# Kernel tuning notes

Measured on AMD Instinct MI355X. Metric: run time of the kernel, lower is better.

Reference implementation:

```python
import jax, jax.numpy as jnp
import numpy as np

B, J, D, W, H, EH, L = 128, 8192, 32, 4, 128, 256, 32
TEMP = 1.0


def _ln(x, g, b, eps=1e-5):
    mu = jnp.mean(x, axis=-1, keepdims=True)
    var = jnp.var(x, axis=-1, keepdims=True)
    return (x - mu) * jax.lax.rsqrt(var + eps) * g + b


def setup_inputs() -> dict:
    key = jax.random.key(0)
    ks = jax.random.split(key, 12)

    def lin(k, fi, fo):
        k1, k2 = jax.random.split(k)
        s = 1.0 / np.sqrt(fi)
        return (jax.random.uniform(k1, (fi, fo), minval=-s, maxval=s, dtype=jnp.float32),
                jax.random.uniform(k2, (fo,), minval=-s, maxval=s, dtype=jnp.float32))

    h_w1, h_b1 = lin(ks[0], 1 + D, H)
    h_w2, h_b2 = lin(ks[1], H, D)
    g_w1, g_b1 = lin(ks[2], D, D // 2)
    g_w2, g_b2 = lin(ks[3], D // 2, W)
    c_w, c_b = lin(ks[4], W * D, D)
    e_w1, e_b1 = lin(ks[5], D, EH)
    e_w2, e_b2 = lin(ks[6], EH, 2 * L)
    return {
        'x': jax.random.normal(ks[7], (B, J), dtype=jnp.float32),
        'mask': jax.random.randint(ks[8], (B, J), 0, 2, dtype=jnp.int32),
        'fe': jax.random.normal(ks[9], (J, D), dtype=jnp.float32),
        'h_w1': h_w1, 'h_b1': h_b1,
        'h_ln1_w': jnp.ones((H,), jnp.float32), 'h_ln1_b': jnp.zeros((H,), jnp.float32),
        'h_w2': h_w2, 'h_b2': h_b2,
        'h_ln2_w': jnp.ones((D,), jnp.float32), 'h_ln2_b': jnp.zeros((D,), jnp.float32),
        'g_w1': g_w1, 'g_b1': g_b1, 'g_w2': g_w2, 'g_b2': g_b2,
        'c_w': c_w, 'c_b': c_b,
        'c_ln_w': jnp.ones((D,), jnp.float32), 'c_ln_b': jnp.zeros((D,), jnp.float32),
        'e_w1': e_w1, 'e_b1': e_b1,
        'e_ln1_w': jnp.ones((EH,), jnp.float32), 'e_ln1_b': jnp.zeros((EH,), jnp.float32),
        'e_w2': e_w2, 'e_b2': e_b2,
        'e_ln2_w': jnp.ones((2 * L,), jnp.float32), 'e_ln2_b': jnp.zeros((2 * L,), jnp.float32),
    }


def _forward(x, mask, fe, h_w1, h_b1, h_ln1_w, h_ln1_b, h_w2, h_b2, h_ln2_w, h_ln2_b,
             g_w1, g_b1, g_w2, g_b2, c_w, c_b, c_ln_w, c_ln_b,
             e_w1, e_b1, e_ln1_w, e_ln1_b, e_w2, e_b2, e_ln2_w, e_ln2_b):
    relu = jax.nn.relu
    # h_in = concat([x, F]) @ h_w1 split into scalar column + shared embedding part
    # (fe @ h_w1[1:]) is [J,H], shared across cells -> avoids materializing [B,J,1+D]
    pre = x[..., None] * h_w1[0][None, None, :] + (fe @ h_w1[1:])[None] + h_b1  # [B,J,H]
    h1 = relu(_ln(pre, h_ln1_w, h_ln1_b))
    h_out = relu(_ln(h1 @ h_w2 + h_b2, h_ln2_w, h_ln2_b))  # [B,J,D]
    raw_gates = relu(h_out @ g_w1 + g_b1) @ g_w2 + g_b2  # [B,J,W]
    logits = jnp.clip(raw_gates * TEMP, -10.0, 10.0)
    logits = jnp.where(mask[..., None] > 0, logits, -1e9)  # masked gather -> -inf fill
    weights = jax.nn.softmax(logits, axis=1)  # softmax over observed junctions
    head_sums = jnp.einsum('bjw,bjd->bwd', weights, h_out)  # [B,W,D]
    comb = relu(_ln(head_sums.reshape(head_sums.shape[0], -1) @ c_w + c_b, c_ln_w, c_ln_b))
    comb = jnp.where((jnp.sum(mask, axis=1) > 0)[:, None], comb, 0.0)  # zero cells -> zeros
    h = relu(_ln(comb @ e_w1 + e_b1, e_ln1_w, e_ln1_b))
    o = relu(_ln(h @ e_w2 + e_b2, e_ln2_w, e_ln2_b))
    mu, logvar = jnp.split(o, 2, axis=-1)
    return mu, logvar


def reference(x, mask, fe, h_w1, h_b1, h_ln1_w, h_ln1_b, h_w2, h_b2, h_ln2_w, h_ln2_b,
              g_w1, g_b1, g_w2, g_b2, c_w, c_b, c_ln_w, c_ln_b,
              e_w1, e_b1, e_ln1_w, e_ln1_b, e_w2, e_b2, e_ln2_w, e_ln2_b):
    return _forward(x, mask, fe, h_w1, h_b1, h_ln1_w, h_ln1_b, h_w2, h_b2, h_ln2_w, h_ln2_b,
                    g_w1, g_b1, g_w2, g_b2, c_w, c_b, c_ln_w, c_ln_b,
                    e_w1, e_b1, e_ln1_w, e_ln1_b, e_w2, e_b2, e_ln2_w, e_ln2_b)
```

## Files before the change

### kernel.cpp

```cpp
#include <hip/hip_runtime.h>
#include <cstdint>

#define BDIM 128
#define JDIM 8192

typedef short s8x __attribute__((ext_vector_type(8)));
typedef float f4x __attribute__((ext_vector_type(4)));
typedef float f2x __attribute__((ext_vector_type(2)));

__device__ __forceinline__ unsigned short bf16u(float f) {
    return __builtin_bit_cast(unsigned short, (__bf16)f);
}
__device__ __forceinline__ unsigned int pkbf(float lo, float hi) {
    return (unsigned int)bf16u(lo) | ((unsigned int)bf16u(hi) << 16);
}
__device__ __forceinline__ f2x upk(unsigned int w) {
    f2x r;
    r.x = __uint_as_float(w << 16);
    r.y = __uint_as_float(w & 0xffff0000u);
    return r;
}
__device__ __forceinline__ f2x pkfma(f2x a, f2x b, f2x c) {
    return __builtin_elementwise_fma(a, b, c);
}
__device__ __forceinline__ f2x pkmax0(f2x a) {
    f2x z = {0.f, 0.f};
    return __builtin_elementwise_max(a, z);
}

__device__ __forceinline__ float allred16(float x) {
    float t;
    asm("v_add_f32 %0, %1, %1 quad_perm:[1,0,3,2] row_mask:0xf bank_mask:0xf"
        : "=v"(t) : "v"(x));
    asm("v_add_f32 %0, %1, %1 quad_perm:[2,3,0,1] row_mask:0xf bank_mask:0xf"
        : "=v"(x) : "v"(t));
    asm("v_add_f32 %0, %1, %1 row_half_mirror row_mask:0xf bank_mask:0xf"
        : "=v"(t) : "v"(x));
    asm("v_add_f32 %0, %1, %1 row_mirror row_mask:0xf bank_mask:0xf"
        : "=v"(x) : "v"(t));
    return x;
}

__global__ __launch_bounds__(128) void k_prep(
    const float* __restrict__ fe, const float* __restrict__ hw1,
    const float* __restrict__ hb1,
    const float* __restrict__ hw2, const float* __restrict__ gw1,
    unsigned short* __restrict__ feWb, float* __restrict__ aux,
    float* __restrict__ scal, uint4* __restrict__ fragW)
{
    const int h = threadIdx.x;
    __shared__ float red[2][3];
    const int wv = h >> 6, ln = h & 63;
    float w1r[32];
#pragma unroll
    for (int d = 0; d < 32; ++d) w1r[d] = hw1[(1 + d) * 128 + h];
    const float hb = hb1[h];
    const float w0h = hw1[h];

    for (int q = 0; q < 8; ++q) {
        const int j = blockIdx.x * 8 + q;
        float acc = hb;
#pragma unroll
        for (int d = 0; d < 32; ++d) acc = fmaf(fe[j * 32 + d], w1r[d], acc);
        feWb[(size_t)j * 128 + h] = bf16u(acc);

        float s1 = acc, sx = w0h * acc, s2 = acc * acc;
#pragma unroll
        for (int m = 1; m <= 32; m <<= 1) {
            s1 += __shfl_xor(s1, m); sx += __shfl_xor(sx, m); s2 += __shfl_xor(s2, m);
        }
        if (q) __syncthreads();
        if (ln == 0) { red[wv][0] = s1; red[wv][1] = sx; red[wv][2] = s2; }
        __syncthreads();
        if (h == 0) {
            aux[j * 4 + 0] = (red[0][0] + red[1][0]) * (1.f / 128.f);
            aux[j * 4 + 1] = (red[0][1] + red[1][1]) * (1.f / 128.f);
            aux[j * 4 + 2] = (red[0][2] + red[1][2]) * (1.f / 128.f);
        }
    }

    if (blockIdx.x == 0) {
        float a = w0h, b = w0h * w0h;
#pragma unroll
        for (int m = 1; m <= 32; m <<= 1) { a += __shfl_xor(a, m); b += __shfl_xor(b, m); }
        __syncthreads();
        if (ln == 0) { red[wv][0] = a; red[wv][1] = b; }
        __syncthreads();
        if (h == 0) {
            scal[0] = (red[0][0] + red[1][0]) * (1.f / 128.f);
            scal[1] = (red[0][1] + red[1][1]) * (1.f / 128.f);
        }
        if (h < 64) {
            const int cc = h & 15, gg = h >> 4;
#pragma unroll
            for (int nt = 0; nt < 2; ++nt)
#pragma unroll
                for (int t = 0; t < 4; ++t) {
                    const int kb = 32 * t + 8 * gg, n = 16 * nt + cc;
                    uint4 u;
                    u.x = pkbf(hw2[(kb + 0) * 32 + n], hw2[(kb + 1) * 32 + n]);
                    u.y = pkbf(hw2[(kb + 2) * 32 + n], hw2[(kb + 3) * 32 + n]);
                    u.z = pkbf(hw2[(kb + 4) * 32 + n], hw2[(kb + 5) * 32 + n]);
                    u.w = pkbf(hw2[(kb + 6) * 32 + n], hw2[(kb + 7) * 32 + n]);
                    fragW[(nt * 4 + t) * 64 + h] = u;
                }
            uint4 u;
            u.x = pkbf(gw1[(8 * gg + 0) * 16 + cc], gw1[(8 * gg + 1) * 16 + cc]);
            u.y = pkbf(gw1[(8 * gg + 2) * 16 + cc], gw1[(8 * gg + 3) * 16 + cc]);
            u.z = pkbf(gw1[(8 * gg + 4) * 16 + cc], gw1[(8 * gg + 5) * 16 + cc]);
            u.w = pkbf(gw1[(8 * gg + 6) * 16 + cc], gw1[(8 * gg + 7) * 16 + cc]);
            fragW[8 * 64 + h] = u;
        }
    }
}

template <int JPW>
__global__ __launch_bounds__(256, 2) void k_main(
    const float* __restrict__ x, const int* __restrict__ mask,
    const unsigned short* __restrict__ feWb, const float* __restrict__ aux,
    const float* __restrict__ scal, const uint4* __restrict__ fragW,
    const float* __restrict__ hw1, const float* __restrict__ ln1w,
    const float* __restrict__ ln1b,
    const float* __restrict__ hb2,
    const float* __restrict__ ln2w, const float* __restrict__ ln2b,
    const float* __restrict__ gb1,
    const float* __restrict__ gw2, const float* __restrict__ gb2,
    float* __restrict__ P, float* __restrict__ SEb, int njb)
{
    __shared__ float w0s[128], g1s[128], b1s[128];
    __shared__ float holds[8][576];
    __shared__ float hsL[2048];
    __shared__ float seL[64];

    const int tid = threadIdx.x, l = tid & 63;
    const int wv = __builtin_amdgcn_readfirstlane(tid >> 6);
    const int c = l & 15, g = l >> 4;
    const int bt = blockIdx.y, bx = blockIdx.x;
    const int b0 = bt * 16;

    if (tid < 128) { w0s[tid] = hw1[tid]; g1s[tid] = ln1w[tid]; b1s[tid] = ln1b[tid]; }
    __syncthreads();

    const float mw0 = scal[0], q0 = scal[1];

    s8x wf[2][4];
#pragma unroll
    for (int nt = 0; nt < 2; ++nt)
#pragma unroll
        for (int t = 0; t < 4; ++t)
            wf[nt][t] = __builtin_bit_cast(s8x, fragW[(nt * 4 + t) * 64 + l]);
    const s8x g1f = __builtin_bit_cast(s8x, fragW[8 * 64 + l]);

    const float hb2a = hb2[c],      hb2b = hb2[16 + c];
    const float g2a  = ln2w[c],     g2b  = ln2w[16 + c];
    const float z2a  = ln2b[c],     z2b  = ln2b[16 + c];
    const float gb1c = gb1[c];
    const float L2E  = 1.442695040888963f;
    float gw2c[4], gb2l[4];
#pragma unroll
    for (int w = 0; w < 4; ++w) {
        gw2c[w] = gw2[c * 4 + w];
        gb2l[w] = fmaf(gb2[w], L2E, -10.f * L2E);
    }

    const int j0 = (bx * 4 + wv) * JPW;
    const float* xrow = x + (size_t)(b0 + c) * JDIM;
    const int*   mrow = mask + (size_t)(b0 + c) * JDIM;

    f2x   hsacc[4][4];
    float seacc[4][4];
#pragma unroll
    for (int r = 0; r < 4; ++r)
#pragma unroll
        for (int w = 0; w < 4; ++w) {
            hsacc[r][w].x = 0.f; hsacc[r][w].y = 0.f; seacc[r][w] = 0.f;
        }

    for (int jp = 0; jp < JPW / 2; ++jp) {
        const int jb = j0 + jp * 2;

        float xv[2], rsv[2], nms[2]; int mv[2];
#pragma unroll
        for (int p = 0; p < 2; ++p) {
            xv[p] = xrow[jb + p];
            mv[p] = mrow[jb + p];
            const float4 au = *(const float4*)(aux + (size_t)(jb + p) * 4);
            const float mu = fmaf(xv[p], mw0, au.x);
            const float e2 = fmaf(xv[p] * xv[p], q0, fmaf(2.f * xv[p], au.y, au.z));
            rsv[p] = rsqrtf(e2 - mu * mu + 1e-5f);
            nms[p] = -mu * rsv[p];
        }

        f4x ca[2], cb[2];
#pragma unroll
        for (int p = 0; p < 2; ++p) { ca[p] = f4x{0.f,0.f,0.f,0.f}; cb[p] = f4x{0.f,0.f,0.f,0.f}; }
#pragma unroll
        for (int p = 0; p < 2; ++p) {
            const f2x xv2 = {xv[p], xv[p]}, rs2 = {rsv[p], rsv[p]}, nm2 = {nms[p], nms[p]};
            const unsigned short* fj = feWb + (size_t)(jb + p) * 128;
#pragma unroll
            for (int t = 0; t < 4; ++t) {
                const int kb = 32 * t + 8 * g;
                const uint4 fw = *(const uint4*)(fj + kb);
                const unsigned int fwv[4] = {fw.x, fw.y, fw.z, fw.w};
                const f2x* wp = (const f2x*)&w0s[kb];
                const f2x* gp = (const f2x*)&g1s[kb];
                const f2x* bp = (const f2x*)&b1s[kb];
                unsigned int res[4];
#pragma unroll
                for (int q = 0; q < 4; ++q) {
                    f2x h2 = pkfma(xv2, wp[q], upk(fwv[q]));
                    h2 = pkfma(h2, rs2, nm2);
                    h2 = pkfma(h2, gp[q], bp[q]);
                    h2 = pkmax0(h2);
                    res[q] = pkbf(h2.x, h2.y);
                }
                const uint4 u = make_uint4(res[0], res[1], res[2], res[3]);
                const s8x af = __builtin_bit_cast(s8x, u);
                ca[p] = __builtin_amdgcn_mfma_f32_16x16x32_bf16(af, wf[0][t], ca[p], 0, 0, 0);
                cb[p] = __builtin_amdgcn_mfma_f32_16x16x32_bf16(af, wf[1][t], cb[p], 0, 0, 0);
            }
        }

        float ho0[2][4], ho1[2][4];
#pragma unroll
        for (int p = 0; p < 2; ++p) {
            float v0[4], v1[4], sr[4], qr[4];
#pragma unroll
            for (int r = 0; r < 4; ++r) {
                v0[r] = ca[p][r] + hb2a;
                v1[r] = cb[p][r] + hb2b;
                sr[r] = v0[r] + v1[r];
                qr[r] = v0[r] * v0[r] + v1[r] * v1[r];
            }
#pragma unroll
            for (int r = 0; r < 4; ++r) { sr[r] = allred16(sr[r]); qr[r] = allred16(qr[r]); }
#pragma unroll
            for (int r = 0; r < 4; ++r) {
                const float m2   = sr[r] * 0.03125f;
                const float rs2b = rsqrtf(fmaf(qr[r], 0.03125f, -m2 * m2) + 1e-5f);
                const float nm2b = -m2 * rs2b;
                ho0[p][r] = fmaxf(fmaf(fmaf(v0[r], rs2b, nm2b), g2a, z2a), 0.f);
                ho1[p][r] = fmaxf(fmaf(fmaf(v1[r], rs2b, nm2b), g2b, z2b), 0.f);
            }
        }

#pragma unroll
        for (int p = 0; p < 2; ++p) {
            float* hp = &holds[wv * 2 + p][0];
#pragma unroll
            for (int r = 0; r < 4; ++r) {
                hp[(4 * g + r) * 36 + c]      = ho0[p][r];
                hp[(4 * g + r) * 36 + 16 + c] = ho1[p][r];
            }
        }
        asm volatile("s_waitcnt lgkmcnt(0)" ::: "memory");
        f4x gc[2];
#pragma unroll
        for (int p = 0; p < 2; ++p) {
            const float* hp = &holds[wv * 2 + p][0];
            const float4 ra  = *(const float4*)&hp[c * 36 + 8 * g];
            const float4 rb2 = *(const float4*)&hp[c * 36 + 8 * g + 4];
            uint4 ua;
            ua.x = pkbf(ra.x, ra.y);   ua.y = pkbf(ra.z, ra.w);
            ua.z = pkbf(rb2.x, rb2.y); ua.w = pkbf(rb2.z, rb2.w);
            const s8x af2 = __builtin_bit_cast(s8x, ua);
            f4x z = {0.f, 0.f, 0.f, 0.f};
            gc[p] = __builtin_amdgcn_mfma_f32_16x16x32_bf16(af2, g1f, z, 0, 0, 0);
        }

#pragma unroll
        for (int p = 0; p < 2; ++p) {
            float pw[16];
#pragma unroll
            for (int r = 0; r < 4; ++r) {
                const float g1r = fmaxf(gc[p][r] + gb1c, 0.f);
#pragma unroll
                for (int w = 0; w < 4; ++w) pw[r * 4 + w] = g1r * gw2c[w];
            }
#pragma unroll
            for (int i = 0; i < 16; ++i) pw[i] = allred16(pw[i]);

            const unsigned bm = (unsigned)__ballot(mv[p] > 0);
            float fm[4];
#pragma unroll
            for (int r = 0; r < 4; ++r) fm[r] = (float)((bm >> (4 * g + r)) & 1u);

#pragma unroll
            for (int r = 0; r < 4; ++r) {
                const f2x ho2 = {ho0[p][r], ho1[p][r]};
#pragma unroll
                for (int w = 0; w < 4; ++w) {
                    float t = fmaf(pw[r * 4 + w], L2E, gb2l[w]);
                    t = __builtin_amdgcn_fmed3f(t, -20.f * L2E, 0.f);
                    const float e = fm[r] * __builtin_amdgcn_exp2f(t);
                    seacc[r][w] += e;
                    const f2x e2v = {e, e};
                    hsacc[r][w] = pkfma(e2v, ho2, hsacc[r][w]);
                }
            }
        }
    }

    for (int ww = 0; ww < 4; ++ww) {
        __syncthreads();
        if (wv == ww) {
#pragma unroll
            for (int r = 0; r < 4; ++r)
#pragma unroll
                for (int w = 0; w < 4; ++w)
#pragma unroll
                    for (int nt = 0; nt < 2; ++nt) {
                        const int idx = ((4 * g + r) * 4 + w) * 32 + c + 16 * nt;
                        const float val = nt ? hsacc[r][w].y : hsacc[r][w].x;
                        if (ww == 0) hsL[idx] = val;
                        else         hsL[idx] += val;
                    }
            if (c == 0) {
#pragma unroll
                for (int r = 0; r < 4; ++r)
#pragma unroll
                    for (int w = 0; w < 4; ++w) {
                        const int si = (4 * g + r) * 4 + w;
                        if (ww == 0) seL[si] = seacc[r][w];
                        else         seL[si] += seacc[r][w];
                    }
            }
        }
    }
    __syncthreads();
    const size_t base = ((size_t)bt * njb + bx) * 2048;
    for (int i = tid; i < 2048; i += 256) P[base + i] = hsL[i];
    if (tid < 64) SEb[((size_t)bt * njb + bx) * 64 + tid] = seL[tid];
}

__global__ __launch_bounds__(128) void k_tail(
    const float* __restrict__ P, const float* __restrict__ SEb,
    const float* __restrict__ cw, const float* __restrict__ cbv,
    const float* __restrict__ clnw, const float* __restrict__ clnb,
    const float* __restrict__ ew1, const float* __restrict__ eb1,
    const float* __restrict__ l1w, const float* __restrict__ l1b,
    const float* __restrict__ ew2, const float* __restrict__ eb2,
    const float* __restrict__ l2w, const float* __restrict__ l2b,
    float* __restrict__ out, int njb)
{
    const int b = blockIdx.x, t = threadIdx.x;
    const int bt = b >> 4, bi = b & 15;
    __shared__ float hsLs[128], combL[32], hL[256], seW[4], sred[64], red[4];

    const float* Pb = P + (size_t)bt * njb * 2048 + bi * 128;
    float sacc = 0.f;
#pragma unroll 4
    for (int jc = 0; jc < njb; ++jc) sacc += Pb[(size_t)jc * 2048 + t];

    if (t < 64) {
        const int w = t & 3, part = t >> 2;
        float sp = 0.f;
        for (int q = part; q < njb; q += 16)
            sp += SEb[((size_t)bt * njb + q) * 64 + bi * 4 + w];
        sred[t] = sp;
    }
    __syncthreads();
    if (t < 4) {
        float v = 0.f;
#pragma unroll
        for (int sl = 0; sl < 16; ++sl) v += sred[sl * 4 + t];
        seW[t] = v;
    }
    __syncthreads();
    const bool has = seW[0] > 0.f;
    hsLs[t] = has ? sacc / seW[t >> 5] : 0.f;
    __syncthreads();

    if (t < 32) {
        float cv = cbv[t];
#pragma unroll 4
        for (int f = 0; f < 128; ++f) cv = fmaf(hsLs[f], cw[f * 32 + t], cv);
        float s = cv, q = cv * cv;
#pragma unroll
        for (int m = 1; m <= 16; m <<= 1) { s += __shfl_xor(s, m); q += __shfl_xor(q, m); }
        const float mu = s * (1.f / 32.f);
        const float rsg = rsqrtf(fmaf(q, 1.f / 32.f, -mu * mu) + 1e-5f);
        const float v = fmaf(fmaf(cv, rsg, -mu * rsg), clnw[t], clnb[t]);
        combL[t] = has ? fmaxf(v, 0.f) : 0.f;
    }
    __syncthreads();

    float h0 = eb1[t], h1v = eb1[t + 128];
#pragma unroll 4
    for (int d = 0; d < 32; ++d) {
        const float cd = combL[d];
        h0  = fmaf(cd, ew1[d * 256 + t], h0);
        h1v = fmaf(cd, ew1[d * 256 + t + 128], h1v);
    }
    {
        float s = h0 + h1v, q = h0 * h0 + h1v * h1v;
#pragma unroll
        for (int m = 1; m <= 32; m <<= 1) { s += __shfl_xor(s, m); q += __shfl_xor(q, m); }
        const int wv = t >> 6, ln = t & 63;
        if (ln == 0) { red[wv * 2] = s; red[wv * 2 + 1] = q; }
    }
    __syncthreads();
    {
        const float S = red[0] + red[2], Q = red[1] + red[3];
        const float mu1 = S * (1.f / 256.f);
        const float rs1 = rsqrtf(fmaf(Q, 1.f / 256.f, -mu1 * mu1) + 1e-5f);
        hL[t]       = fmaxf(fmaf(fmaf(h0,  rs1, -mu1 * rs1), l1w[t],       l1b[t]),       0.f);
        hL[t + 128] = fmaxf(fmaf(fmaf(h1v, rs1, -mu1 * rs1), l1w[t + 128], l1b[t + 128]), 0.f);
    }
    __syncthreads();

    if (t < 64) {
        float ov = eb2[t];
#pragma unroll 4
        for (int m = 0; m < 256; ++m) ov = fmaf(hL[m], ew2[m * 64 + t], ov);
        float s = ov, q = ov * ov;
#pragma unroll
        for (int m = 1; m <= 32; m <<= 1) { s += __shfl_xor(s, m); q += __shfl_xor(q, m); }
        const float mu2 = s * (1.f / 64.f);
        const float rs2 = rsqrtf(fmaf(q, 1.f / 64.f, -mu2 * mu2) + 1e-5f);
        const float o = fmaxf(fmaf(fmaf(ov, rs2, -mu2 * rs2), l2w[t], l2b[t]), 0.f);
        if (t < 32) out[b * 32 + t] = o;
        else        out[4096 + b * 32 + (t - 32)] = o;
    }
}

extern "C" void kernel_launch(void* const* d_in, const int* in_sizes, int n_in,
                              void* d_out, int out_size, void* d_ws, size_t ws_size,
                              hipStream_t stream)
{
    (void)in_sizes; (void)n_in; (void)out_size;
    const float* x    = (const float*)d_in[0];
    const int*   mask = (const int*)d_in[1];
    const float* fe   = (const float*)d_in[2];
    const float* hw1  = (const float*)d_in[3];
    const float* hb1  = (const float*)d_in[4];
    const float* ln1w = (const float*)d_in[5];
    const float* ln1b = (const float*)d_in[6];
    const float* hw2  = (const float*)d_in[7];
    const float* hb2  = (const float*)d_in[8];
    const float* ln2w = (const float*)d_in[9];
    const float* ln2b = (const float*)d_in[10];
    const float* gw1  = (const float*)d_in[11];
    const float* gb1  = (const float*)d_in[12];
    const float* gw2  = (const float*)d_in[13];
    const float* gb2  = (const float*)d_in[14];
    const float* cw   = (const float*)d_in[15];
    const float* cbv  = (const float*)d_in[16];
    const float* clnw = (const float*)d_in[17];
    const float* clnb = (const float*)d_in[18];
    const float* ew1  = (const float*)d_in[19];
    const float* eb1  = (const float*)d_in[20];
    const float* l1w  = (const float*)d_in[21];
    const float* l1b  = (const float*)d_in[22];
    const float* ew2  = (const float*)d_in[23];
    const float* eb2  = (const float*)d_in[24];
    const float* l2w  = (const float*)d_in[25];
    const float* l2b  = (const float*)d_in[26];

    const size_t fragOff = (2u << 20) + (128u << 10) + 256u;
    const size_t base    = fragOff + 9u * 64u * 16u;
    int NJB = 128;
    {
        const size_t need = base + (size_t)8 * 128 * 2048 * 4 + (size_t)8 * 128 * 64 * 4;
        if (ws_size < need) NJB = 64;
    }

    char* ws = (char*)d_ws;
    unsigned short* feWb = (unsigned short*)ws;
    float* aux   = (float*)(ws + (2u << 20));
    float* scal  = (float*)(ws + (2u << 20) + (128u << 10));
    uint4* fragW = (uint4*)(ws + fragOff);
    float* P     = (float*)(ws + base);
    float* SEb   = (float*)(ws + base + (size_t)8 * NJB * 2048 * 4);

    hipLaunchKernelGGL(k_prep, dim3(JDIM / 8), dim3(128), 0, stream,
                       fe, hw1, hb1, hw2, gw1, feWb, aux, scal, fragW);
    if (NJB == 128)
        hipLaunchKernelGGL((k_main<16>), dim3(128, 8), dim3(256), 0, stream,
                           x, mask, feWb, aux, scal, fragW,
                           hw1, ln1w, ln1b, hb2, ln2w, ln2b,
                           gb1, gw2, gb2, P, SEb, 128);
    else
        hipLaunchKernelGGL((k_main<32>), dim3(64, 8), dim3(256), 0, stream,
                           x, mask, feWb, aux, scal, fragW,
                           hw1, ln1w, ln1b, hb2, ln2w, ln2b,
                           gb1, gw2, gb2, P, SEb, 64);
    hipLaunchKernelGGL(k_tail, dim3(BDIM), dim3(128), 0, stream,
                       P, SEb, cw, cbv, clnw, clnb,
                       ew1, eb1, l1w, l1b, ew2, eb2, l2w, l2b,
                       (float*)d_out, NJB);
}
```

Before: 237.3 us.

## Remap MFMA rows to 4 cells by 4 junctions and shrink partial buffers

The 16 MFMA rows per wave now hold 4 batch cells times 4 consecutive junctions, instead of 16 cells sharing one junction. Each block covers 4 cells and 256 junctions over a 32x32 grid, so each wave keeps only 4 head accumulators. The per-block partial head sums and exp sums shrink to 512 and 16 floats, with 32 partials per cell. This cuts partial-buffer writes and the tail's reduction reads, and makes x and mask loads more contiguous. In exchange, each feature-embedding row is reused by 4 cells instead of 16, so embedding loads rise, and the workspace-size fallback path is removed.

```diff
diff --git a/kernel.cpp b/kernel.cpp
--- a/kernel.cpp
+++ b/kernel.cpp
@@ -114,7 +114,6 @@
     }
 }
 
-template <int JPW>
 __global__ __launch_bounds__(256, 2) void k_main(
     const float* __restrict__ x, const int* __restrict__ mask,
     const unsigned short* __restrict__ feWb, const float* __restrict__ aux,
@@ -125,18 +124,19 @@
     const float* __restrict__ ln2w, const float* __restrict__ ln2b,
     const float* __restrict__ gb1,
     const float* __restrict__ gw2, const float* __restrict__ gb2,
-    float* __restrict__ P, float* __restrict__ SEb, int njb)
+    float* __restrict__ P, float* __restrict__ SEb)
 {
     __shared__ float w0s[128], g1s[128], b1s[128];
     __shared__ float holds[8][576];
-    __shared__ float hsL[2048];
-    __shared__ float seL[64];
+    __shared__ float hsL[512];
+    __shared__ float seL[16];
 
     const int tid = threadIdx.x, l = tid & 63;
     const int wv = __builtin_amdgcn_readfirstlane(tid >> 6);
     const int c = l & 15, g = l >> 4;
     const int bt = blockIdx.y, bx = blockIdx.x;
-    const int b0 = bt * 16;
+    const int b0 = bt * 4;
+    const int cell_in = c >> 2, jsub = c & 3;
 
     if (tid < 128) { w0s[tid] = hw1[tid]; g1s[tid] = ln1w[tid]; b1s[tid] = ln1b[tid]; }
     __syncthreads();
@@ -163,141 +163,112 @@
         gb2l[w] = fmaf(gb2[w], L2E, -10.f * L2E);
     }
 
-    const int j0 = (bx * 4 + wv) * JPW;
-    const float* xrow = x + (size_t)(b0 + c) * JDIM;
-    const int*   mrow = mask + (size_t)(b0 + c) * JDIM;
-
-    f2x   hsacc[4][4];
-    float seacc[4][4];
-#pragma unroll
-    for (int r = 0; r < 4; ++r)
-#pragma unroll
-        for (int w = 0; w < 4; ++w) {
-            hsacc[r][w].x = 0.f; hsacc[r][w].y = 0.f; seacc[r][w] = 0.f;
-        }
-
-    for (int jp = 0; jp < JPW / 2; ++jp) {
-        const int jb = j0 + jp * 2;
-
-        float xv[2], rsv[2], nms[2]; int mv[2];
-#pragma unroll
-        for (int p = 0; p < 2; ++p) {
-            xv[p] = xrow[jb + p];
-            mv[p] = mrow[jb + p];
-            const float4 au = *(const float4*)(aux + (size_t)(jb + p) * 4);
-            const float mu = fmaf(xv[p], mw0, au.x);
-            const float e2 = fmaf(xv[p] * xv[p], q0, fmaf(2.f * xv[p], au.y, au.z));
-            rsv[p] = rsqrtf(e2 - mu * mu + 1e-5f);
-            nms[p] = -mu * rsv[p];
-        }
-
-        f4x ca[2], cb[2];
-#pragma unroll
-        for (int p = 0; p < 2; ++p) { ca[p] = f4x{0.f,0.f,0.f,0.f}; cb[p] = f4x{0.f,0.f,0.f,0.f}; }
-#pragma unroll
-        for (int p = 0; p < 2; ++p) {
-            const f2x xv2 = {xv[p], xv[p]}, rs2 = {rsv[p], rsv[p]}, nm2 = {nms[p], nms[p]};
-            const unsigned short* fj = feWb + (size_t)(jb + p) * 128;
-#pragma unroll
-            for (int t = 0; t < 4; ++t) {
-                const int kb = 32 * t + 8 * g;
-                const uint4 fw = *(const uint4*)(fj + kb);
-                const unsigned int fwv[4] = {fw.x, fw.y, fw.z, fw.w};
-                const f2x* wp = (const f2x*)&w0s[kb];
-                const f2x* gp = (const f2x*)&g1s[kb];
-                const f2x* bp = (const f2x*)&b1s[kb];
-                unsigned int res[4];
-#pragma unroll
-                for (int q = 0; q < 4; ++q) {
-                    f2x h2 = pkfma(xv2, wp[q], upk(fwv[q]));
-                    h2 = pkfma(h2, rs2, nm2);
-                    h2 = pkfma(h2, gp[q], bp[q]);
-                    h2 = pkmax0(h2);
-                    res[q] = pkbf(h2.x, h2.y);
-                }
-                const uint4 u = make_uint4(res[0], res[1], res[2], res[3]);
-                const s8x af = __builtin_bit_cast(s8x, u);
-                ca[p] = __builtin_amdgcn_mfma_f32_16x16x32_bf16(af, wf[0][t], ca[p], 0, 0, 0);
-                cb[p] = __builtin_amdgcn_mfma_f32_16x16x32_bf16(af, wf[1][t], cb[p], 0, 0, 0);
+    const int j0 = (bx * 4 + wv) * 64;
+    const float* xrow = x + (size_t)(b0 + cell_in) * JDIM;
+    const int*   mrow = mask + (size_t)(b0 + cell_in) * JDIM;
+
+    f2x   hsacc[4];
+    float seacc[4];
+#pragma unroll
+    for (int w = 0; w < 4; ++w) { hsacc[w].x = 0.f; hsacc[w].y = 0.f; seacc[w] = 0.f; }
+
+    for (int bi = 0; bi < 16; ++bi) {
+        const int jb = j0 + bi * 4;
+        const int j  = jb + jsub;
+
+        const float xv = xrow[j];
+        const int   mv = mrow[j];
+        const float4 au = *(const float4*)(aux + (size_t)j * 4);
+        const float mu = fmaf(xv, mw0, au.x);
+        const float e2 = fmaf(xv * xv, q0, fmaf(2.f * xv, au.y, au.z));
+        const float rs = rsqrtf(e2 - mu * mu + 1e-5f);
+        const float nms = -mu * rs;
+        const f2x xv2 = {xv, xv}, rs2 = {rs, rs}, nm2 = {nms, nms};
+
+        f4x ca = {0.f, 0.f, 0.f, 0.f}, cb = {0.f, 0.f, 0.f, 0.f};
+        const unsigned short* fj = feWb + (size_t)j * 128;
+#pragma unroll
+        for (int t = 0; t < 4; ++t) {
+            const int kb = 32 * t + 8 * g;
+            const uint4 fw = *(const uint4*)(fj + kb);
+            const unsigned int fwv[4] = {fw.x, fw.y, fw.z, fw.w};
+            const f2x* wp = (const f2x*)&w0s[kb];
+            const f2x* gp = (const f2x*)&g1s[kb];
+            const f2x* bp = (const f2x*)&b1s[kb];
+            unsigned int res[4];
+#pragma unroll
+            for (int q = 0; q < 4; ++q) {
+                f2x h2 = pkfma(xv2, wp[q], upk(fwv[q]));
+                h2 = pkfma(h2, rs2, nm2);
+                h2 = pkfma(h2, gp[q], bp[q]);
+                h2 = pkmax0(h2);
+                res[q] = pkbf(h2.x, h2.y);
             }
-        }
-
-        float ho0[2][4], ho1[2][4];
-#pragma unroll
-        for (int p = 0; p < 2; ++p) {
-            float v0[4], v1[4], sr[4], qr[4];
-#pragma unroll
-            for (int r = 0; r < 4; ++r) {
-                v0[r] = ca[p][r] + hb2a;
-                v1[r] = cb[p][r] + hb2b;
-                sr[r] = v0[r] + v1[r];
-                qr[r] = v0[r] * v0[r] + v1[r] * v1[r];
-            }
-#pragma unroll
-            for (int r = 0; r < 4; ++r) { sr[r] = allred16(sr[r]); qr[r] = allred16(qr[r]); }
-#pragma unroll
-            for (int r = 0; r < 4; ++r) {
-                const float m2   = sr[r] * 0.03125f;
-                const float rs2b = rsqrtf(fmaf(qr[r], 0.03125f, -m2 * m2) + 1e-5f);
-                const float nm2b = -m2 * rs2b;
-                ho0[p][r] = fmaxf(fmaf(fmaf(v0[r], rs2b, nm2b), g2a, z2a), 0.f);
-                ho1[p][r] = fmaxf(fmaf(fmaf(v1[r], rs2b, nm2b), g2b, z2b), 0.f);
-            }
-        }
-
-#pragma unroll
-        for (int p = 0; p < 2; ++p) {
-            float* hp = &holds[wv * 2 + p][0];
-#pragma unroll
-            for (int r = 0; r < 4; ++r) {
-                hp[(4 * g + r) * 36 + c]      = ho0[p][r];
-                hp[(4 * g + r) * 36 + 16 + c] = ho1[p][r];
-            }
+            const uint4 u = make_uint4(res[0], res[1], res[2], res[3]);
+            const s8x af = __builtin_bit_cast(s8x, u);
+            ca = __builtin_amdgcn_mfma_f32_16x16x32_bf16(af, wf[0][t], ca, 0, 0, 0);
+            cb = __builtin_amdgcn_mfma_f32_16x16x32_bf16(af, wf[1][t], cb, 0, 0, 0);
+        }
+
+        float v0[4], v1[4], sr[4], qr[4];
+#pragma unroll
+        for (int r = 0; r < 4; ++r) {
+            v0[r] = ca[r] + hb2a;
+            v1[r] = cb[r] + hb2b;
+            sr[r] = v0[r] + v1[r];
+            qr[r] = v0[r] * v0[r] + v1[r] * v1[r];
+        }
+#pragma unroll
+        for (int r = 0; r < 4; ++r) { sr[r] = allred16(sr[r]); qr[r] = allred16(qr[r]); }
+        float ho0[4], ho1[4];
+#pragma unroll
+        for (int r = 0; r < 4; ++r) {
+            const float m2   = sr[r] * 0.03125f;
+            const float rs2b = rsqrtf(fmaf(qr[r], 0.03125f, -m2 * m2) + 1e-5f);
+            const float nm2b = -m2 * rs2b;
+            ho0[r] = fmaxf(fmaf(fmaf(v0[r], rs2b, nm2b), g2a, z2a), 0.f);
+            ho1[r] = fmaxf(fmaf(fmaf(v1[r], rs2b, nm2b), g2b, z2b), 0.f);
+        }
+
+        float* hp = &holds[wv * 2 + (bi & 1)][0];
+#pragma unroll
+        for (int r = 0; r < 4; ++r) {
+            hp[(4 * g + r) * 36 + c]      = ho0[r];
+            hp[(4 * g + r) * 36 + 16 + c] = ho1[r];
         }
         asm volatile("s_waitcnt lgkmcnt(0)" ::: "memory");
-        f4x gc[2];
-#pragma unroll
-        for (int p = 0; p < 2; ++p) {
-            const float* hp = &holds[wv * 2 + p][0];
-            const float4 ra  = *(const float4*)&hp[c * 36 + 8 * g];
-            const float4 rb2 = *(const float4*)&hp[c * 36 + 8 * g + 4];
-            uint4 ua;
-            ua.x = pkbf(ra.x, ra.y);   ua.y = pkbf(ra.z, ra.w);
-            ua.z = pkbf(rb2.x, rb2.y); ua.w = pkbf(rb2.z, rb2.w);
-            const s8x af2 = __builtin_bit_cast(s8x, ua);
-            f4x z = {0.f, 0.f, 0.f, 0.f};
-            gc[p] = __builtin_amdgcn_mfma_f32_16x16x32_bf16(af2, g1f, z, 0, 0, 0);
-        }
-
-#pragma unroll
-        for (int p = 0; p < 2; ++p) {
-            float pw[16];
-#pragma unroll
-            for (int r = 0; r < 4; ++r) {
-                const float g1r = fmaxf(gc[p][r] + gb1c, 0.f);
-#pragma unroll
-                for (int w = 0; w < 4; ++w) pw[r * 4 + w] = g1r * gw2c[w];
-            }
-#pragma unroll
-            for (int i = 0; i < 16; ++i) pw[i] = allred16(pw[i]);
-
-            const unsigned bm = (unsigned)__ballot(mv[p] > 0);
-            float fm[4];
-#pragma unroll
-            for (int r = 0; r < 4; ++r) fm[r] = (float)((bm >> (4 * g + r)) & 1u);
-
-#pragma unroll
-            for (int r = 0; r < 4; ++r) {
-                const f2x ho2 = {ho0[p][r], ho1[p][r]};
-#pragma unroll
-                for (int w = 0; w < 4; ++w) {
-                    float t = fmaf(pw[r * 4 + w], L2E, gb2l[w]);
-                    t = __builtin_amdgcn_fmed3f(t, -20.f * L2E, 0.f);
-                    const float e = fm[r] * __builtin_amdgcn_exp2f(t);
-                    seacc[r][w] += e;
-                    const f2x e2v = {e, e};
-                    hsacc[r][w] = pkfma(e2v, ho2, hsacc[r][w]);
-                }
+        const float4 ra  = *(const float4*)&hp[c * 36 + 8 * g];
+        const float4 rb2 = *(const float4*)&hp[c * 36 + 8 * g + 4];
+        uint4 ua;
+        ua.x = pkbf(ra.x, ra.y);   ua.y = pkbf(ra.z, ra.w);
+        ua.z = pkbf(rb2.x, rb2.y); ua.w = pkbf(rb2.z, rb2.w);
+        const s8x af2 = __builtin_bit_cast(s8x, ua);
+        f4x zz = {0.f, 0.f, 0.f, 0.f};
+        const f4x gc = __builtin_amdgcn_mfma_f32_16x16x32_bf16(af2, g1f, zz, 0, 0, 0);
+
+        float pw[16];
+#pragma unroll
+        for (int r = 0; r < 4; ++r) {
+            const float g1r = fmaxf(gc[r] + gb1c, 0.f);
+#pragma unroll
+            for (int w = 0; w < 4; ++w) pw[r * 4 + w] = g1r * gw2c[w];
+        }
+#pragma unroll
+        for (int i = 0; i < 16; ++i) pw[i] = allred16(pw[i]);
+
+        const unsigned long long bm = __ballot(mv > 0);
+#pragma unroll
+        for (int r = 0; r < 4; ++r) {
+            const float fm = (float)((bm >> (4 * g + r)) & 1ull);
+            const f2x ho2 = {ho0[r], ho1[r]};
+#pragma unroll
+            for (int w = 0; w < 4; ++w) {
+                float t2 = fmaf(pw[r * 4 + w], L2E, gb2l[w]);
+                t2 = __builtin_amdgcn_fmed3f(t2, -20.f * L2E, 0.f);
+                const float e = fm * __builtin_amdgcn_exp2f(t2);
+                seacc[w] += e;
+                const f2x e2v = {e, e};
+                hsacc[w] = pkfma(e2v, ho2, hsacc[w]);
             }
         }
     }
@@ -306,32 +277,28 @@
         __syncthreads();
         if (wv == ww) {
 #pragma unroll
-            for (int r = 0; r < 4; ++r)
-#pragma unroll
-                for (int w = 0; w < 4; ++w)
-#pragma unroll
-                    for (int nt = 0; nt < 2; ++nt) {
-                        const int idx = ((4 * g + r) * 4 + w) * 32 + c + 16 * nt;
-                        const float val = nt ? hsacc[r][w].y : hsacc[r][w].x;
-                        if (ww == 0) hsL[idx] = val;
-                        else         hsL[idx] += val;
-                    }
+            for (int w = 0; w < 4; ++w)
+#pragma unroll
+                for (int nt = 0; nt < 2; ++nt) {
+                    const int idx = (g * 4 + w) * 32 + 16 * nt + c;
+                    const float val = nt ? hsacc[w].y : hsacc[w].x;
+                    if (ww == 0) hsL[idx] = val;
+                    else         hsL[idx] += val;
+                }
             if (c == 0) {
 #pragma unroll
-                for (int r = 0; r < 4; ++r)
-#pragma unroll
-                    for (int w = 0; w < 4; ++w) {
-                        const int si = (4 * g + r) * 4 + w;
-                        if (ww == 0) seL[si] = seacc[r][w];
-                        else         seL[si] += seacc[r][w];
-                    }
+                for (int w = 0; w < 4; ++w) {
+                    const int si = g * 4 + w;
+                    if (ww == 0) seL[si] = seacc[w];
+                    else         seL[si] += seacc[w];
+                }
             }
         }
     }
     __syncthreads();
-    const size_t base = ((size_t)bt * njb + bx) * 2048;
-    for (int i = tid; i < 2048; i += 256) P[base + i] = hsL[i];
-    if (tid < 64) SEb[((size_t)bt * njb + bx) * 64 + tid] = seL[tid];
+    const size_t base = ((size_t)bt * 32 + bx) * 512;
+    for (int i = tid; i < 512; i += 256) P[base + i] = hsL[i];
+    if (tid < 16) SEb[((size_t)bt * 32 + bx) * 16 + tid] = seL[tid];
 }
 
 __global__ __launch_bounds__(128) void k_tail(
@@ -342,30 +309,21 @@
     const float* __restrict__ l1w, const float* __restrict__ l1b,
     const float* __restrict__ ew2, const float* __restrict__ eb2,
     const float* __restrict__ l2w, const float* __restrict__ l2b,
-    float* __restrict__ out, int njb)
+    float* __restrict__ out)
 {
     const int b = blockIdx.x, t = threadIdx.x;
-    const int bt = b >> 4, bi = b & 15;
-    __shared__ float hsLs[128], combL[32], hL[256], seW[4], sred[64], red[4];
-
-    const float* Pb = P + (size_t)bt * njb * 2048 + bi * 128;
+    const int bt = b >> 2, cell = b & 3;
+    __shared__ float hsLs[128], combL[32], hL[256], seW[4], red[4];
+
+    const float* Pb = P + (size_t)bt * 32 * 512 + (size_t)(cell * 4 + (t >> 5)) * 32 + (t & 31);
     float sacc = 0.f;
 #pragma unroll 4
-    for (int jc = 0; jc < njb; ++jc) sacc += Pb[(size_t)jc * 2048 + t];
-
-    if (t < 64) {
-        const int w = t & 3, part = t >> 2;
-        float sp = 0.f;
-        for (int q = part; q < njb; q += 16)
-            sp += SEb[((size_t)bt * njb + q) * 64 + bi * 4 + w];
-        sred[t] = sp;
-    }
-    __syncthreads();
+    for (int q = 0; q < 32; ++q) sacc += Pb[(size_t)q * 512];
+
     if (t < 4) {
-        float v = 0.f;
-#pragma unroll
-        for (int sl = 0; sl < 16; ++sl) v += sred[sl * 4 + t];
-        seW[t] = v;
+        float s = 0.f;
+        for (int q = 0; q < 32; ++q) s += SEb[((size_t)bt * 32 + q) * 16 + cell * 4 + t];
+        seW[t] = s;
     }
     __syncthreads();
     const bool has = seW[0] > 0.f;
@@ -429,7 +387,7 @@
                               void* d_out, int out_size, void* d_ws, size_t ws_size,
                               hipStream_t stream)
 {
-    (void)in_sizes; (void)n_in; (void)out_size;
+    (void)in_sizes; (void)n_in; (void)out_size; (void)ws_size;
     const float* x    = (const float*)d_in[0];
     const int*   mask = (const int*)d_in[1];
     const float* fe   = (const float*)d_in[2];
@@ -459,35 +417,25 @@
     const float* l2b  = (const float*)d_in[26];
 
     const size_t fragOff = (2u << 20) + (128u << 10) + 256u;
-    const size_t base    = fragOff + 9u * 64u * 16u;
-    int NJB = 128;
-    {
-        const size_t need = base + (size_t)8 * 128 * 2048 * 4 + (size_t)8 * 128 * 64 * 4;
-        if (ws_size < need) NJB = 64;
-    }
+    const size_t pOff    = fragOff + 9u * 64u * 16u;
+    const size_t seOff   = pOff + (size_t)32 * 32 * 512 * 4;
 
     char* ws = (char*)d_ws;
     unsigned short* feWb = (unsigned short*)ws;
     float* aux   = (float*)(ws + (2u << 20));
     float* scal  = (float*)(ws + (2u << 20) + (128u << 10));
     uint4* fragW = (uint4*)(ws + fragOff);
-    float* P     = (float*)(ws + base);
-    float* SEb   = (float*)(ws + base + (size_t)8 * NJB * 2048 * 4);
+    float* P     = (float*)(ws + pOff);
+    float* SEb   = (float*)(ws + seOff);
 
     hipLaunchKernelGGL(k_prep, dim3(JDIM / 8), dim3(128), 0, stream,
                        fe, hw1, hb1, hw2, gw1, feWb, aux, scal, fragW);
-    if (NJB == 128)
-        hipLaunchKernelGGL((k_main<16>), dim3(128, 8), dim3(256), 0, stream,
-                           x, mask, feWb, aux, scal, fragW,
-                           hw1, ln1w, ln1b, hb2, ln2w, ln2b,
-                           gb1, gw2, gb2, P, SEb, 128);
-    else
-        hipLaunchKernelGGL((k_main<32>), dim3(64, 8), dim3(256), 0, stream,
-                           x, mask, feWb, aux, scal, fragW,
-                           hw1, ln1w, ln1b, hb2, ln2w, ln2b,
-                           gb1, gw2, gb2, P, SEb, 64);
+    hipLaunchKernelGGL(k_main, dim3(32, 32), dim3(256), 0, stream,
+                       x, mask, feWb, aux, scal, fragW,
+                       hw1, ln1w, ln1b, hb2, ln2w, ln2b,
+                       gb1, gw2, gb2, P, SEb);
     hipLaunchKernelGGL(k_tail, dim3(BDIM), dim3(128), 0, stream,
                        P, SEb, cw, cbv, clnw, clnb,
                        ew1, eb1, l1w, l1b, ew2, eb2, l2w, l2b,
-                       (float*)d_out, NJB);
-}
+                       (float*)d_out);
+}
```

New measurement: 221.5 us. 1.07x faster.
